# Kernel optimization log

Measured on AMD Instinct MI355X. Metric: run time of the kernel, lower is better.

## Reference

```python
import jax, jax.numpy as jnp
import numpy as np

# Static problem constants (see shape_source)
T_, H_, W_ = 8, 37, 37          # frames, feature-map height/width (518/14)
NH, MP = 8, 8                   # num_heads, max_points


def _point_mask_np():
    # n_points(t, r) = max(1, int(MP * (1 - |t-r|/(T-1)))) as in the TxT loop.
    d = np.abs(np.arange(T_)[:, None] - np.arange(T_)[None, :])
    n_p = np.maximum(1, (MP * (1.0 - d / (T_ - 1))).astype(np.int64))
    return np.arange(MP)[None, None, :] < n_p[:, :, None]   # [T, T, P] bool


def setup_inputs() -> dict:
    key = jax.random.key(0)
    ks = jax.random.split(key, 4)
    B, T, N, C = 2, T_, H_ * W_, 384
    f_bt = jax.random.normal(ks[0], (B, T, N, C), jnp.float32)
    Wq = 0.05 * jax.random.normal(ks[1], (C, C), jnp.float32)
    Woff = 0.1 * jax.random.normal(ks[2], (C, NH * MP * 2), jnp.float32)  # offsets span a few pixels
    Wout = 0.05 * jax.random.normal(ks[3], (C, C), jnp.float32)
    return {
        'f_bt': f_bt,
        'Wq': Wq, 'bq': jnp.zeros((C,), jnp.float32),
        'Woff': Woff, 'boff': jnp.zeros((NH * MP * 2,), jnp.float32),
        'Wout': Wout, 'bout': jnp.zeros((C,), jnp.float32),
    }


def _forward(f_bt, Wq, bq, Woff, boff, Wout, bout):
    B, T, N, C = f_bt.shape
    h, P = NH, MP
    hd = C // h
    scale = hd ** -0.5
    H, W = H_, W_

    # Per-frame projections (query and offsets depend only on t, computed once).
    q = (f_bt @ Wq + bq).reshape(B, T, N, h, hd)                 # [B,T,N,h,hd]
    off = (f_bt @ Woff + boff).reshape(B, T, N, h, P, 2)         # [B,T,N,h,P,2]

    ys, xs = jnp.meshgrid(jnp.arange(H), jnp.arange(W), indexing='ij')
    coords = jnp.stack([ys, xs], -1).reshape(N, 2).astype(f_bt.dtype)
    # Sampling locations in pixel space (align_corners=True normalize+denormalize is identity).
    loc = coords[None, None, :, None, None, :] + off             # [B,T,N,h,P,2]

    # Reference frames as per-head channel images, flattened spatially.
    ref = f_bt.transpose(0, 1, 3, 2).reshape(B, T, h, hd, N)     # [B,T,h,hd,H*W]
    mask = jnp.asarray(_point_mask_np())                         # [T,T,P]

    def attend(q_t, loc_t, mask_t):
        # q_t: [B,N,h,hd], loc_t: [B,N,h,P,2], mask_t: [T,P]
        y = loc_t[..., 0]
        x = loc_t[..., 1]
        y0f = jnp.floor(y)
        x0f = jnp.floor(x)
        wy = y - y0f
        wx = x - x0f

        def gather(yf, xf, w):
            yi = yf.astype(jnp.int32)
            xi = xf.astype(jnp.int32)
            valid = ((yi >= 0) & (yi < H) & (xi >= 0) & (xi < W)).astype(q_t.dtype)
            idx = jnp.clip(yi, 0, H - 1) * W + jnp.clip(xi, 0, W - 1)     # [B,N,h,P]
            idx = idx.transpose(0, 2, 1, 3).reshape(B, 1, h, 1, N * P)
            idx = jnp.broadcast_to(idx, (B, T, h, 1, N * P))
            vals = jnp.take_along_axis(ref, idx, axis=4)                   # [B,T,h,hd,N*P]
            vals = vals.reshape(B, T, h, hd, N, P)
            wv = (w * valid).transpose(0, 2, 1, 3)[:, None, :, None, :, :]  # [B,1,h,1,N,P]
            return vals * wv

        # Bilinear sample (zeros padding) of every reference frame at the
        # offset-predicted points of frame t.
        s = (gather(y0f, x0f, (1 - wy) * (1 - wx))
             + gather(y0f, x0f + 1, (1 - wy) * wx)
             + gather(y0f + 1, x0f, wy * (1 - wx))
             + gather(y0f + 1, x0f + 1, wy * wx))                # [B,T,h,hd,N,P]

        logits = jnp.einsum('bnhd,brhdnp->brnhp', q_t, s) * scale
        logits = logits + jnp.where(mask_t[None, :, None, None, :], 0.0, -1e30)
        attn = jax.nn.softmax(logits, axis=-1)
        out = jnp.einsum('brnhp,brhdnp->brnhd', attn, s).mean(axis=1)  # avg over T refs
        return out.reshape(B, N, C) @ Wout + bout

    body = jax.checkpoint(attend)

    def step(carry, xs):
        q_t, loc_t, mask_t = xs
        return carry, body(q_t, loc_t, mask_t)

    _, fused = jax.lax.scan(
        step, None,
        (q.transpose(1, 0, 2, 3, 4), loc.transpose(1, 0, 2, 3, 4, 5), mask))
    return fused.transpose(1, 0, 2, 3)   # [B,T,N,C]


def reference(f_bt, Wq, bq, Woff, boff, Wout, bout):
    return _forward(f_bt, Wq, bq, Woff, boff, Wout, bout)
```

## Files before the change

kernel.cpp:

```cpp
#include <hip/hip_runtime.h>
#include <hip/hip_bf16.h>
#include <cstddef>

constexpr int B_  = 2;
constexpr int T_  = 8;
constexpr int HW_ = 37;
constexpr int N_  = HW_ * HW_;
constexpr int C_  = 384;
constexpr int NH_ = 8;
constexpr int MP_ = 8;
constexpr int HD_ = C_ / NH_;
constexpr int M_  = B_ * T_ * N_;

typedef short bf16x8 __attribute__((ext_vector_type(8)));
typedef float f32x4 __attribute__((ext_vector_type(4)));
typedef float f32x2 __attribute__((ext_vector_type(2)));

static __device__ __forceinline__ unsigned short bf16_bits(float v) {
  __hip_bfloat16 b = __float2bfloat16(v);
  return *reinterpret_cast<unsigned short*>(&b);
}

static __device__ __forceinline__ f32x2 unpk(unsigned u) {
  f32x2 r;
  r.x = __uint_as_float(u << 16);
  r.y = __uint_as_float(u & 0xffff0000u);
  return r;
}

__global__ __launch_bounds__(256)
void cast_a_kernel(const float* __restrict__ f, __hip_bfloat16* __restrict__ A16) {
  int i = blockIdx.x * 256 + threadIdx.x;
  float4 v = ((const float4*)f)[i];
  ushort4 o;
  o.x = bf16_bits(v.x); o.y = bf16_bits(v.y);
  o.z = bf16_bits(v.z); o.w = bf16_bits(v.w);
  ((ushort4*)A16)[i] = o;
}

__global__ __launch_bounds__(256)
void prep_w_kernel(const float* __restrict__ Wq, const float* __restrict__ Woff,
                   const float* __restrict__ Wout,
                   __hip_bfloat16* __restrict__ Wt, __hip_bfloat16* __restrict__ Wot) {
  int nrow = blockIdx.x;
  if (nrow < 512) {
    const float* src; int col, ld;
    if (nrow < 384) { src = Wq; col = nrow; ld = 384; }
    else            { src = Woff; col = nrow - 384; ld = 128; }
    for (int k = threadIdx.x; k < 384; k += 256)
      Wt[(size_t)nrow * 384 + k] = __float2bfloat16(src[(size_t)k * ld + col]);
  } else {
    int col = nrow - 512;
    for (int k = threadIdx.x; k < 384; k += 256)
      Wot[(size_t)col * 384 + k] = __float2bfloat16(Wout[(size_t)k * 384 + col]);
  }
}

__global__ __launch_bounds__(256)
void transpose_cast_kernel(const float* __restrict__ f,
                           __hip_bfloat16* __restrict__ ft) {
  const int bn = blockIdx.x;
  const int n = bn % N_;
  const int b = bn / N_;
  const size_t dst_base = (size_t)bn * (T_ * C_);
#pragma unroll
  for (int i = 0; i < 12; ++i) {
    int idx = i * 256 + threadIdx.x;
    int t = idx / C_;
    int c = idx - t * C_;
    float v = f[((size_t)(b * T_ + t) * N_ + n) * C_ + c];
    ft[dst_base + idx] = __float2bfloat16(v);
  }
}

__global__ __launch_bounds__(256)
void mfma_gemm_kernel(const __hip_bfloat16* __restrict__ A,
                      const __hip_bfloat16* __restrict__ Wt,
                      const float* __restrict__ b0, const float* __restrict__ b1,
                      float* __restrict__ out0, float* __restrict__ out1,
                      int split, float out0_scale) {
  __shared__ __hip_bfloat16 As[128][40];
  __shared__ __hip_bfloat16 Bs[128][40];
  const int m0 = blockIdx.x * 128;
  const int n0 = blockIdx.y * 128;
  const int tid = threadIdx.x;
  const int wv = tid >> 6, lane = tid & 63;
  const int wr = wv >> 1, wc = wv & 1;
  const int lr = lane & 15, kg = lane >> 4;

  f32x4 acc[4][4] = {};

  for (int k0 = 0; k0 < 384; k0 += 32) {
#pragma unroll
    for (int u = 0; u < 2; ++u) {
      int c = tid + u * 256;
      int row = c >> 2;
      int off = (c & 3) * 8;
      int gm = m0 + row;
      uint4 va = make_uint4(0u, 0u, 0u, 0u);
      if (gm < M_) va = *(const uint4*)(A + (size_t)gm * 384 + k0 + off);
      *(uint4*)&As[row][off] = va;
      uint4 vb = *(const uint4*)(Wt + (size_t)(n0 + row) * 384 + k0 + off);
      *(uint4*)&Bs[row][off] = vb;
    }
    __syncthreads();

    bf16x8 af[4], bfr[4];
#pragma unroll
    for (int i = 0; i < 4; ++i)
      af[i] = *(const bf16x8*)&As[wr * 64 + i * 16 + lr][kg * 8];
#pragma unroll
    for (int i = 0; i < 4; ++i)
      bfr[i] = *(const bf16x8*)&Bs[wc * 64 + i * 16 + lr][kg * 8];

#pragma unroll
    for (int mi = 0; mi < 4; ++mi)
#pragma unroll
      for (int ni = 0; ni < 4; ++ni)
        acc[mi][ni] = __builtin_amdgcn_mfma_f32_16x16x32_bf16(
            af[mi], bfr[ni], acc[mi][ni], 0, 0, 0);
    __syncthreads();
  }

  const int mrow = (lane >> 4) * 4;
#pragma unroll
  for (int mi = 0; mi < 4; ++mi) {
#pragma unroll
    for (int ni = 0; ni < 4; ++ni) {
#pragma unroll
      for (int j = 0; j < 4; ++j) {
        int gm = m0 + wr * 64 + mi * 16 + mrow + j;
        int gn = n0 + wc * 64 + ni * 16 + lr;
        if (gm >= M_) continue;
        float v = acc[mi][ni][j];
        if (!split) {
          out0[(size_t)gm * 384 + gn] = (v + b0[gn]) * out0_scale;
        } else {
          if (gn < 384) out0[(size_t)gm * 384 + gn] = (v + b0[gn]) * out0_scale;
          else          out1[(size_t)gm * 128 + (gn - 384)] = v + b1[gn - 384];
        }
      }
    }
  }
}

__global__ __launch_bounds__(256)
void attend_kernel(const __hip_bfloat16* __restrict__ ft,
                   const float* __restrict__ Q,
                   const float* __restrict__ OFF,
                   __hip_bfloat16* __restrict__ O1) {
  const int grid = B_ * N_ * 2;
  const int q8 = grid / 8, r8 = grid % 8;
  int c = blockIdx.x & 7, j = blockIdx.x >> 3;
  int id = (c < r8) ? c * (q8 + 1) + j : r8 * (q8 + 1) + (c - r8) * q8 + j;
  const int hq = id & 1;
  const int bn = id >> 1;

  const int n = bn % N_;
  const int b = bn / N_;
  const int w    = threadIdx.x >> 6;
  const int h    = hq * 4 + w;
  const int lane = threadIdx.x & 63;
  const int p = lane >> 3;
  const int k = lane & 7;
  const float cy = (float)(n / HW_);
  const float cx = (float)(n % HW_);
  const int bnb = b * N_;
  const int chb = h * HD_ + 6 * k;

  for (int t = 0; t < T_; ++t) {
    const size_t row = (size_t)(b * T_ + t) * N_ + n;

    const f32x2* qp = (const f32x2*)(Q + row * C_ + h * HD_ + 6 * k);
    f32x2 q01 = qp[0], q23 = qp[1], q45 = qp[2];

    const float* op = OFF + row * (NH_ * MP_ * 2) + h * (MP_ * 2) + p * 2;
    float y = cy + op[0];
    float x = cx + op[1];
    float y0f = floorf(y), x0f = floorf(x);
    float wy = y - y0f, wx = x - x0f;
    int y0 = (int)y0f, x0 = (int)x0f;
    int y1 = y0 + 1, x1 = x0 + 1;
    float vy0 = (y0 >= 0 && y0 < HW_) ? 1.f : 0.f;
    float vy1 = (y1 >= 0 && y1 < HW_) ? 1.f : 0.f;
    float vx0 = (x0 >= 0 && x0 < HW_) ? 1.f : 0.f;
    float vx1 = (x1 >= 0 && x1 < HW_) ? 1.f : 0.f;
    int cy0 = min(max(y0, 0), HW_ - 1), cy1 = min(max(y1, 0), HW_ - 1);
    int cx0 = min(max(x0, 0), HW_ - 1), cx1 = min(max(x1, 0), HW_ - 1);
    float tw0 = (1.f - wy) * (1.f - wx) * vy0 * vx0;
    float tw1 = (1.f - wy) * wx * vy0 * vx1;
    float tw2 = wy * (1.f - wx) * vy1 * vx0;
    float tw3 = wy * wx * vy1 * vx1;
    f32x2 tw0v = {tw0, tw0}, tw1v = {tw1, tw1}, tw2v = {tw2, tw2}, tw3v = {tw3, tw3};

    int base0 = ((bnb + cy0 * HW_ + cx0) * T_) * C_ + chb;
    int base1 = ((bnb + cy0 * HW_ + cx1) * T_) * C_ + chb;
    int base2 = ((bnb + cy1 * HW_ + cx0) * T_) * C_ + chb;
    int base3 = ((bnb + cy1 * HW_ + cx1) * T_) * C_ + chb;

    f32x2 oa01 = {0.f, 0.f}, oa23 = {0.f, 0.f}, oa45 = {0.f, 0.f};

#pragma unroll
    for (int r = 0; r < T_; ++r) {
      const int roff = r * C_;
      const unsigned* ta = (const unsigned*)(ft + base0 + roff);
      const unsigned* tb = (const unsigned*)(ft + base1 + roff);
      const unsigned* tc = (const unsigned*)(ft + base2 + roff);
      const unsigned* td = (const unsigned*)(ft + base3 + roff);
      unsigned ua0 = ta[0], ua1 = ta[1], ua2 = ta[2];
      unsigned ub0 = tb[0], ub1 = tb[1], ub2 = tb[2];
      unsigned uc0 = tc[0], uc1 = tc[1], uc2 = tc[2];
      unsigned ud0 = td[0], ud1 = td[1], ud2 = td[2];

      f32x2 s01 = unpk(ua0) * tw0v + unpk(ub0) * tw1v + unpk(uc0) * tw2v + unpk(ud0) * tw3v;
      f32x2 s23 = unpk(ua1) * tw0v + unpk(ub1) * tw1v + unpk(uc1) * tw2v + unpk(ud1) * tw3v;
      f32x2 s45 = unpk(ua2) * tw0v + unpk(ub2) * tw1v + unpk(uc2) * tw2v + unpk(ud2) * tw3v;

      f32x2 lg2 = q01 * s01 + q23 * s23 + q45 * s45;
      float lg = lg2.x + lg2.y;
      lg += __shfl_xor(lg, 1);
      lg += __shfl_xor(lg, 2);
      lg += __shfl_xor(lg, 4);

      int dd = t - r; dd = dd < 0 ? -dd : dd;
      int npts = (56 - 8 * dd) / 7; npts = npts < 1 ? 1 : npts;

      float e = (p < npts) ? __expf(lg) : 0.f;
      float ssum = e;
      ssum += __shfl_xor(ssum, 8);
      ssum += __shfl_xor(ssum, 16);
      ssum += __shfl_xor(ssum, 32);
      float attn = e * __builtin_amdgcn_rcpf(ssum);
      f32x2 attnv = {attn, attn};

      oa01 += attnv * s01;
      oa23 += attnv * s23;
      oa45 += attnv * s45;
    }

    oa01.x += __shfl_xor(oa01.x, 8); oa01.x += __shfl_xor(oa01.x, 16); oa01.x += __shfl_xor(oa01.x, 32);
    oa01.y += __shfl_xor(oa01.y, 8); oa01.y += __shfl_xor(oa01.y, 16); oa01.y += __shfl_xor(oa01.y, 32);
    oa23.x += __shfl_xor(oa23.x, 8); oa23.x += __shfl_xor(oa23.x, 16); oa23.x += __shfl_xor(oa23.x, 32);
    oa23.y += __shfl_xor(oa23.y, 8); oa23.y += __shfl_xor(oa23.y, 16); oa23.y += __shfl_xor(oa23.y, 32);
    oa45.x += __shfl_xor(oa45.x, 8); oa45.x += __shfl_xor(oa45.x, 16); oa45.x += __shfl_xor(oa45.x, 32);
    oa45.y += __shfl_xor(oa45.y, 8); oa45.y += __shfl_xor(oa45.y, 16); oa45.y += __shfl_xor(oa45.y, 32);

    if (p == 0) {
      __hip_bfloat16* outp = O1 + row * C_ + h * HD_ + 6 * k;
      unsigned* u = (unsigned*)outp;
      u[0] = (unsigned)bf16_bits(oa01.x * 0.125f) | ((unsigned)bf16_bits(oa01.y * 0.125f) << 16);
      u[1] = (unsigned)bf16_bits(oa23.x * 0.125f) | ((unsigned)bf16_bits(oa23.y * 0.125f) << 16);
      u[2] = (unsigned)bf16_bits(oa45.x * 0.125f) | ((unsigned)bf16_bits(oa45.y * 0.125f) << 16);
    }
  }
}

extern "C" void kernel_launch(void* const* d_in, const int* in_sizes, int n_in,
                              void* d_out, int out_size, void* d_ws, size_t ws_size,
                              hipStream_t stream) {
  const float* f    = (const float*)d_in[0];
  const float* Wq   = (const float*)d_in[1];
  const float* bq   = (const float*)d_in[2];
  const float* Woff = (const float*)d_in[3];
  const float* boff = (const float*)d_in[4];
  const float* Wout = (const float*)d_in[5];
  const float* bout = (const float*)d_in[6];
  float* outp = (float*)d_out;

  float* Qbuf = (float*)d_ws;
  float* OFFb = Qbuf + (size_t)M_ * C_;
  __hip_bfloat16* ft  = (__hip_bfloat16*)(OFFb + (size_t)M_ * 128);
  __hip_bfloat16* A16 = ft + (size_t)B_ * N_ * T_ * C_;
  __hip_bfloat16* O1  = A16;
  __hip_bfloat16* Wt  = A16 + (size_t)M_ * C_;
  __hip_bfloat16* Wot = Wt + (size_t)512 * 384;

  dim3 blk(256);

  cast_a_kernel<<<dim3((M_ * C_) / 4 / 256), blk, 0, stream>>>(f, A16);
  prep_w_kernel<<<dim3(896), blk, 0, stream>>>(Wq, Woff, Wout, Wt, Wot);
  transpose_cast_kernel<<<dim3(B_ * N_), blk, 0, stream>>>(f, ft);

  mfma_gemm_kernel<<<dim3((M_ + 127) / 128, 4), blk, 0, stream>>>(
      A16, Wt, bq, boff, Qbuf, OFFb, 1, 0.144337567297406441f);

  attend_kernel<<<dim3(B_ * N_ * 2), blk, 0, stream>>>(ft, Qbuf, OFFb, O1);

  mfma_gemm_kernel<<<dim3((M_ + 127) / 128, 3), blk, 0, stream>>>(
      O1, Wot, bout, nullptr, outp, nullptr, 0, 1.0f);
}
```

Baseline: 316.1 us.

## Swap lane mapping so cross-lane reductions use DPP and swizzle; process two refs per iteration

Lanes are remapped so the 8 points sit in adjacent lanes and the 8 channel groups are strided, so the per-point softmax sum and final point reduction use DPP row ops and ds_swizzle instead of full cross-lane shuffles. The reference-frame loop is unrolled two frames at a time to give more independent loads and math in flight. exp is replaced with exp2f by folding log2(e) into the query scale in the projection GEMM. A launch-bounds occupancy hint is added, and the larger unrolled body risks higher register pressure.

```diff
diff --git a/kernel.cpp b/kernel.cpp
--- a/kernel.cpp
+++ b/kernel.cpp
@@ -26,6 +26,25 @@
   r.x = __uint_as_float(u << 16);
   r.y = __uint_as_float(u & 0xffff0000u);
   return r;
+}
+
+static __device__ __forceinline__ float dpp_add1(float v) {
+  int t = __builtin_amdgcn_update_dpp(0, __float_as_int(v), 0xB1, 0xF, 0xF, true);
+  return v + __int_as_float(t);
+}
+static __device__ __forceinline__ float dpp_add2(float v) {
+  int t = __builtin_amdgcn_update_dpp(0, __float_as_int(v), 0x4E, 0xF, 0xF, true);
+  return v + __int_as_float(t);
+}
+#define SWZ_XOR4(v)  __int_as_float(__builtin_amdgcn_ds_swizzle(__float_as_int(v), 0x101F))
+#define SWZ_XOR8(v)  __int_as_float(__builtin_amdgcn_ds_swizzle(__float_as_int(v), 0x201F))
+#define SWZ_XOR16(v) __int_as_float(__builtin_amdgcn_ds_swizzle(__float_as_int(v), 0x401F))
+
+static __device__ __forceinline__ float p_reduce(float v) {
+  v = dpp_add1(v);
+  v = dpp_add2(v);
+  v = v + SWZ_XOR4(v);
+  return v;
 }
 
 __global__ __launch_bounds__(256)
@@ -144,7 +163,7 @@
   }
 }
 
-__global__ __launch_bounds__(256)
+__global__ __launch_bounds__(256, 8)
 void attend_kernel(const __hip_bfloat16* __restrict__ ft,
                    const float* __restrict__ Q,
                    const float* __restrict__ OFF,
@@ -161,8 +180,8 @@
   const int w    = threadIdx.x >> 6;
   const int h    = hq * 4 + w;
   const int lane = threadIdx.x & 63;
-  const int p = lane >> 3;
-  const int k = lane & 7;
+  const int p = lane & 7;
+  const int k = lane >> 3;
   const float cy = (float)(n / HW_);
   const float cx = (float)(n % HW_);
   const int bnb = b * N_;
@@ -193,57 +212,68 @@
     float tw3 = wy * wx * vy1 * vx1;
     f32x2 tw0v = {tw0, tw0}, tw1v = {tw1, tw1}, tw2v = {tw2, tw2}, tw3v = {tw3, tw3};
 
-    int base0 = ((bnb + cy0 * HW_ + cx0) * T_) * C_ + chb;
-    int base1 = ((bnb + cy0 * HW_ + cx1) * T_) * C_ + chb;
-    int base2 = ((bnb + cy1 * HW_ + cx0) * T_) * C_ + chb;
-    int base3 = ((bnb + cy1 * HW_ + cx1) * T_) * C_ + chb;
+    const unsigned* tp0 = (const unsigned*)(ft + ((bnb + cy0 * HW_ + cx0) * T_) * C_ + chb) + 4 * 192;
+    const unsigned* tp1 = (const unsigned*)(ft + ((bnb + cy0 * HW_ + cx1) * T_) * C_ + chb) + 4 * 192;
+    const unsigned* tp2 = (const unsigned*)(ft + ((bnb + cy1 * HW_ + cx0) * T_) * C_ + chb) + 4 * 192;
+    const unsigned* tp3 = (const unsigned*)(ft + ((bnb + cy1 * HW_ + cx1) * T_) * C_ + chb) + 4 * 192;
 
     f32x2 oa01 = {0.f, 0.f}, oa23 = {0.f, 0.f}, oa45 = {0.f, 0.f};
 
 #pragma unroll
-    for (int r = 0; r < T_; ++r) {
-      const int roff = r * C_;
-      const unsigned* ta = (const unsigned*)(ft + base0 + roff);
-      const unsigned* tb = (const unsigned*)(ft + base1 + roff);
-      const unsigned* tc = (const unsigned*)(ft + base2 + roff);
-      const unsigned* td = (const unsigned*)(ft + base3 + roff);
-      unsigned ua0 = ta[0], ua1 = ta[1], ua2 = ta[2];
-      unsigned ub0 = tb[0], ub1 = tb[1], ub2 = tb[2];
-      unsigned uc0 = tc[0], uc1 = tc[1], uc2 = tc[2];
-      unsigned ud0 = td[0], ud1 = td[1], ud2 = td[2];
-
-      f32x2 s01 = unpk(ua0) * tw0v + unpk(ub0) * tw1v + unpk(uc0) * tw2v + unpk(ud0) * tw3v;
-      f32x2 s23 = unpk(ua1) * tw0v + unpk(ub1) * tw1v + unpk(uc1) * tw2v + unpk(ud1) * tw3v;
-      f32x2 s45 = unpk(ua2) * tw0v + unpk(ub2) * tw1v + unpk(uc2) * tw2v + unpk(ud2) * tw3v;
-
-      f32x2 lg2 = q01 * s01 + q23 * s23 + q45 * s45;
-      float lg = lg2.x + lg2.y;
-      lg += __shfl_xor(lg, 1);
-      lg += __shfl_xor(lg, 2);
-      lg += __shfl_xor(lg, 4);
-
-      int dd = t - r; dd = dd < 0 ? -dd : dd;
-      int npts = (56 - 8 * dd) / 7; npts = npts < 1 ? 1 : npts;
-
-      float e = (p < npts) ? __expf(lg) : 0.f;
-      float ssum = e;
-      ssum += __shfl_xor(ssum, 8);
-      ssum += __shfl_xor(ssum, 16);
-      ssum += __shfl_xor(ssum, 32);
-      float attn = e * __builtin_amdgcn_rcpf(ssum);
-      f32x2 attnv = {attn, attn};
-
-      oa01 += attnv * s01;
-      oa23 += attnv * s23;
-      oa45 += attnv * s45;
+    for (int hf = 0; hf < 4; ++hf) {
+      const int rA = 2 * hf, rB = rA + 1;
+      const int oA = (rA - 4) * 192, oB = (rB - 4) * 192;
+
+      unsigned a0A = tp0[oA + 0], a1A = tp0[oA + 1], a2A = tp0[oA + 2];
+      unsigned b0A = tp1[oA + 0], b1A = tp1[oA + 1], b2A = tp1[oA + 2];
+      unsigned c0A = tp2[oA + 0], c1A = tp2[oA + 1], c2A = tp2[oA + 2];
+      unsigned d0A = tp3[oA + 0], d1A = tp3[oA + 1], d2A = tp3[oA + 2];
+      unsigned a0B = tp0[oB + 0], a1B = tp0[oB + 1], a2B = tp0[oB + 2];
+      unsigned b0B = tp1[oB + 0], b1B = tp1[oB + 1], b2B = tp1[oB + 2];
+      unsigned c0B = tp2[oB + 0], c1B = tp2[oB + 1], c2B = tp2[oB + 2];
+      unsigned d0B = tp3[oB + 0], d1B = tp3[oB + 1], d2B = tp3[oB + 2];
+
+      f32x2 s01A = unpk(a0A) * tw0v + unpk(b0A) * tw1v + unpk(c0A) * tw2v + unpk(d0A) * tw3v;
+      f32x2 s23A = unpk(a1A) * tw0v + unpk(b1A) * tw1v + unpk(c1A) * tw2v + unpk(d1A) * tw3v;
+      f32x2 s45A = unpk(a2A) * tw0v + unpk(b2A) * tw1v + unpk(c2A) * tw2v + unpk(d2A) * tw3v;
+      f32x2 s01B = unpk(a0B) * tw0v + unpk(b0B) * tw1v + unpk(c0B) * tw2v + unpk(d0B) * tw3v;
+      f32x2 s23B = unpk(a1B) * tw0v + unpk(b1B) * tw1v + unpk(c1B) * tw2v + unpk(d1B) * tw3v;
+      f32x2 s45B = unpk(a2B) * tw0v + unpk(b2B) * tw1v + unpk(c2B) * tw2v + unpk(d2B) * tw3v;
+
+      f32x2 lgA2 = q01 * s01A + q23 * s23A + q45 * s45A;
+      f32x2 lgB2 = q01 * s01B + q23 * s23B + q45 * s45B;
+      float lgA = lgA2.x + lgA2.y;
+      float lgB = lgB2.x + lgB2.y;
+
+      lgA = lgA + SWZ_XOR8(lgA);
+      lgB = lgB + SWZ_XOR8(lgB);
+      lgA = lgA + SWZ_XOR16(lgA);
+      lgB = lgB + SWZ_XOR16(lgB);
+      lgA = lgA + __shfl_xor(lgA, 32);
+      lgB = lgB + __shfl_xor(lgB, 32);
+
+      int ddA = t - rA; ddA = ddA < 0 ? -ddA : ddA;
+      int ddB = t - rB; ddB = ddB < 0 ? -ddB : ddB;
+      int nptsA = (56 - 8 * ddA) / 7; nptsA = nptsA < 1 ? 1 : nptsA;
+      int nptsB = (56 - 8 * ddB) / 7; nptsB = nptsB < 1 ? 1 : nptsB;
+
+      float eA = (p < nptsA) ? exp2f(lgA) : 0.f;
+      float eB = (p < nptsB) ? exp2f(lgB) : 0.f;
+      float sA = dpp_add1(eA); float sB = dpp_add1(eB);
+      sA = dpp_add2(sA);       sB = dpp_add2(sB);
+      sA = sA + SWZ_XOR4(sA);  sB = sB + SWZ_XOR4(sB);
+      float attnA = eA * __builtin_amdgcn_rcpf(sA);
+      float attnB = eB * __builtin_amdgcn_rcpf(sB);
+      f32x2 avA = {attnA, attnA}, avB = {attnB, attnB};
+
+      oa01 += avA * s01A + avB * s01B;
+      oa23 += avA * s23A + avB * s23B;
+      oa45 += avA * s45A + avB * s45B;
     }
 
-    oa01.x += __shfl_xor(oa01.x, 8); oa01.x += __shfl_xor(oa01.x, 16); oa01.x += __shfl_xor(oa01.x, 32);
-    oa01.y += __shfl_xor(oa01.y, 8); oa01.y += __shfl_xor(oa01.y, 16); oa01.y += __shfl_xor(oa01.y, 32);
-    oa23.x += __shfl_xor(oa23.x, 8); oa23.x += __shfl_xor(oa23.x, 16); oa23.x += __shfl_xor(oa23.x, 32);
-    oa23.y += __shfl_xor(oa23.y, 8); oa23.y += __shfl_xor(oa23.y, 16); oa23.y += __shfl_xor(oa23.y, 32);
-    oa45.x += __shfl_xor(oa45.x, 8); oa45.x += __shfl_xor(oa45.x, 16); oa45.x += __shfl_xor(oa45.x, 32);
-    oa45.y += __shfl_xor(oa45.y, 8); oa45.y += __shfl_xor(oa45.y, 16); oa45.y += __shfl_xor(oa45.y, 32);
+    oa01.x = p_reduce(oa01.x); oa01.y = p_reduce(oa01.y);
+    oa23.x = p_reduce(oa23.x); oa23.y = p_reduce(oa23.y);
+    oa45.x = p_reduce(oa45.x); oa45.y = p_reduce(oa45.y);
 
     if (p == 0) {
       __hip_bfloat16* outp = O1 + row * C_ + h * HD_ + 6 * k;
@@ -282,7 +312,7 @@
   transpose_cast_kernel<<<dim3(B_ * N_), blk, 0, stream>>>(f, ft);
 
   mfma_gemm_kernel<<<dim3((M_ + 127) / 128, 4), blk, 0, stream>>>(
-      A16, Wt, bq, boff, Qbuf, OFFb, 1, 0.144337567297406441f);
+      A16, Wt, bq, boff, Qbuf, OFFb, 1, 0.20822825268806912f);
 
   attend_kernel<<<dim3(B_ * N_ * 2), blk, 0, stream>>>(ft, Qbuf, OFFb, O1);
 
```

After: 756.1 us. 2.39x slower.
